# Kernel tuning notes

Measured on AMD Instinct MI355X. Metric: run time of the kernel, lower is better.

## Reference

```python
import jax, jax.numpy as jnp
import numpy as np

N_ATOMS = 10000
N_PAIRS = 320000
C = 64        # channel width (pp_nodes[-1], ii_nodes[-1], pi_nodes[-1])
NB = 10       # n_basis
EPS = 1e-3    # torsion-boost epsilon


def setup_inputs() -> dict:
    key = jax.random.key(0)
    ks = jax.random.split(key, 24)
    f32 = jnp.float32

    def w(k, shp):
        return jax.random.normal(k, shp, f32) / np.float32(np.sqrt(shp[0]))

    ind_2 = jax.random.randint(ks[0], (N_PAIRS, 2), 0, N_ATOMS)
    p1 = jax.random.normal(ks[1], (N_ATOMS, C), f32)
    p3 = jax.random.normal(ks[2], (N_ATOMS, 3, C), f32)
    basis = jax.random.uniform(ks[3], (N_PAIRS, NB), dtype=f32)
    d3 = jax.random.normal(ks[4], (N_PAIRS, 3), f32)
    d3 = d3 / jnp.linalg.norm(d3, axis=-1, keepdims=True)  # unit bond directions
    fc_edge = jax.random.uniform(ks[5], (N_PAIRS, 1), dtype=f32)  # cutoff in [0,1]

    return {
        'ind_2': ind_2, 'p1': p1, 'p3': p3, 'basis': basis, 'd3': d3, 'fc_edge': fc_edge,
        'pp_pre_W1': w(ks[6], (C, C)), 'pp_pre_b1': jnp.zeros((C,), f32),
        'pp_pre_W2': w(ks[7], (C, C)), 'pp_pre_b2': jnp.zeros((C,), f32),
        'pi_W': w(ks[8], (2 * C, C * NB)), 'pi_b': jnp.zeros((C * NB,), f32),
        'ii_W': w(ks[9], (C, 2 * C)),
        'pp_post_W1': w(ks[10], (2 * C, C)), 'pp_post_W2': w(ks[11], (C, C)),
        'eq_pp_W': w(ks[12], (C, C)),
        'pp1_W1': w(ks[13], (2 * C, C)), 'pp1_b1': jnp.zeros((C,), f32),
        'pp1_W2': w(ks[14], (C, 2 * C)), 'pp1_b2': jnp.zeros((2 * C,), f32),
    }


def _gc_block(ind_2, p1, p3, basis, d3, fc_edge,
              pp_pre_W1, pp_pre_b1, pp_pre_W2, pp_pre_b2,
              pi_W, pi_b, ii_W, pp_post_W1, pp_post_W2,
              eq_pp_W, pp1_W1, pp1_b1, pp1_W2, pp1_b2):
    n_atoms = p1.shape[0]
    i = ind_2[:, 0]
    j = ind_2[:, 1]

    # ---- InvarLayer ----
    # pp_pre: FF [C,C], tanh, bias
    p1_in = jnp.tanh(jnp.tanh(p1 @ pp_pre_W1 + pp_pre_b1) @ pp_pre_W2 + pp_pre_b2)
    # PILayer: concat(p1[i], p1[j]) -> Dense(C*NB) -> contract with radial basis
    pair = jnp.concatenate([p1_in[i], p1_in[j]], axis=-1)            # (P, 2C)
    h = jnp.tanh(pair @ pi_W + pi_b).reshape(-1, C, NB)              # (P, C, NB)
    i_pair = jnp.einsum('pcb,pb->pc', h, basis)                      # (P, C)
    # ii: FF [2C] (doubled for n_props=2), tanh, no bias
    i_pair = jnp.tanh(i_pair @ ii_W)                                 # (P, 2C)
    # IP: scatter-add onto receiver atom i
    p1_scat = jax.ops.segment_sum(i_pair, i, num_segments=n_atoms)   # (N, 2C)
    # pp_post: FF [C,C], tanh, no bias
    p1_new = jnp.tanh(jnp.tanh(p1_scat @ pp_post_W1) @ pp_post_W2)   # (N, C)

    i1a, i1b = jnp.split(i_pair, 2, axis=-1)  # chunks; rank-3 branch uses i1s[1]

    # ---- torsion boost (compute_torsion_boost_t3) ----
    v = jax.ops.segment_sum(d3 * fc_edge, i, num_segments=n_atoms)   # (N, 3)
    v_i = v[i]
    proj = jnp.sum(v_i * d3, axis=-1, keepdims=True)
    w = v_i - proj * d3                                              # perpendicular part
    w2 = jnp.sum(w * w, axis=-1, keepdims=True)
    g_deg = w2 / (w2 + (10.0 * EPS) ** 2)
    t3 = w * jax.lax.rsqrt(w2 + EPS * EPS) * g_deg                   # (P, 3)
    tb_gate = g_deg * (fc_edge * fc_edge)                            # (P, 1)

    # ---- EquivarLayer ----
    gate = i1b[:, None, :]                                           # (P, 1, C)
    ix = p3[j] * gate + d3[:, :, None] * gate \
         + t3[:, :, None] * (i1b * tb_gate)[:, None, :]              # (P, 3, C)
    p3_new = jax.ops.segment_sum(ix, i, num_segments=n_atoms)        # (N, 3, C)
    p3_new = p3_new @ eq_pp_W                                        # PP: no bias, no act
    dotted = jnp.einsum('ixr,ixr->ir', p3_new, p3_new)               # (N, C)

    # ---- output PP + gating ----
    h2 = jnp.tanh(jnp.concatenate([p1_new, dotted], axis=-1) @ pp1_W1 + pp1_b1)
    h2 = jnp.tanh(h2 @ pp1_W2 + pp1_b2)                              # (N, 2C)
    g1, g3 = jnp.split(h2, 2, axis=-1)
    p1_out = g1                                                      # (N, C)
    p3_out = p3_new * g3[:, None, :]                                 # ScaleLayer
    return p1_out, p3_out


def reference(ind_2, p1, p3, basis, d3, fc_edge,
              pp_pre_W1, pp_pre_b1, pp_pre_W2, pp_pre_b2,
              pi_W, pi_b, ii_W, pp_post_W1, pp_post_W2,
              eq_pp_W, pp1_W1, pp1_b1, pp1_W2, pp1_b2):
    return _gc_block(ind_2, p1, p3, basis, d3, fc_edge,
                     pp_pre_W1, pp_pre_b1, pp_pre_W2, pp_pre_b2,
                     pi_W, pi_b, ii_W, pp_post_W1, pp_post_W2,
                     eq_pp_W, pp1_W1, pp1_b1, pp1_W2, pp1_b2)
```

## Files before the change

kernel.cpp:

```cpp
#include <hip/hip_runtime.h>
#include <hip/hip_bf16.h>

#define N_ATOMS 10000
#define N_PAIRS 320000
#define C_ 64
#define NB_ 10

typedef short bf16x8 __attribute__((ext_vector_type(8)));
typedef float f32x4 __attribute__((ext_vector_type(4)));

__device__ __forceinline__ float bf2f(__hip_bfloat16 x) { return __bfloat162float(x); }
__device__ __forceinline__ float ldf(const void* p, int i, int isf32) {
    return isf32 ? ((const float*)p)[i] : bf2f(((const __hip_bfloat16*)p)[i]);
}
__device__ __forceinline__ short f2bs(float x) {
    __hip_bfloat16 h = __float2bfloat16(x);
    return *reinterpret_cast<short*>(&h);
}
__device__ __forceinline__ float bs2f(unsigned short s) {
    return __uint_as_float(((unsigned)s) << 16);
}
__device__ __forceinline__ float tanh_fast(float x) {
    const float e = __expf(2.0f * x);
    return 1.0f - 2.0f * __builtin_amdgcn_rcpf(e + 1.0f);
}

#define W_PPREW1 0
#define W_PPREB1 4096
#define W_PPREW2 4160
#define W_PPREB2 8256
#define W_PIW    8320
#define W_PIB    90240
#define W_IIW    90880
#define W_PPOSTW1 99072
#define W_PPOSTW2 107264
#define W_EQW    111360
#define W_Q1W    115456
#define W_Q1B    123648
#define W_Q2W    123712
#define W_Q2B    131904
#define W_TOTAL  132032

__global__ void k_probe(const void* __restrict__ d3, int* __restrict__ flag)
{
    if (threadIdx.x == 0 && blockIdx.x == 0) {
        float sf = 0.f, sb = 0.f;
        const float* f = (const float*)d3;
        const __hip_bfloat16* b = (const __hip_bfloat16*)d3;
        for (int r = 0; r < 4; r++) {
            float x = f[r*3], y = f[r*3+1], z = f[r*3+2];
            float n = x*x + y*y + z*z;
            sf += isfinite(n) ? fabsf(n - 1.f) : 1e30f;
            float xb = bf2f(b[r*3]), yb = bf2f(b[r*3+1]), zb = bf2f(b[r*3+2]);
            float nb = xb*xb + yb*yb + zb*zb;
            sb += isfinite(nb) ? fabsf(nb - 1.f) : 1e30f;
        }
        *flag = (sf < sb) ? 1 : 0;
    }
}

__global__ __launch_bounds__(256) void k_convert(
    const void* s0, const void* s1, const void* s2, const void* s3,
    const void* s4, const void* s5, const void* s6, const void* s7,
    const void* s8, const void* s9, const void* s10, const void* s11,
    const void* s12, const void* s13,
    float* __restrict__ wbuf, const int* __restrict__ flagp)
{
    const int idx = blockIdx.x * 256 + threadIdx.x;
    if (idx >= W_TOTAL) return;
    const int isf32 = *flagp;
    const int offs[15] = {W_PPREW1, W_PPREB1, W_PPREW2, W_PPREB2, W_PIW, W_PIB,
                          W_IIW, W_PPOSTW1, W_PPOSTW2, W_EQW, W_Q1W, W_Q1B,
                          W_Q2W, W_Q2B, W_TOTAL};
    const void* srcs[14] = {s0,s1,s2,s3,s4,s5,s6,s7,s8,s9,s10,s11,s12,s13};
    int t = 0;
    while (idx >= offs[t + 1]) t++;
    wbuf[idx] = ldf(srcs[t], idx - offs[t], isf32);
}

__global__ __launch_bounds__(256) void k_pack(
    const float* __restrict__ wbuf,
    short* __restrict__ piWBh, short* __restrict__ piWBl,
    short* __restrict__ iiWh, short* __restrict__ iiWl)
{
    int idx = blockIdx.x * 256 + threadIdx.x;
    if (idx < 81920) {
        const int j = idx & 7, lane = (idx >> 3) & 63, s = (idx >> 9) & 3, T = idx >> 11;
        const int k = s * 32 + (lane >> 4) * 8 + j;
        const int colp = T * 16 + (lane & 15);
        const int b = colp >> 6, c = colp & 63;
        const float v = wbuf[W_PIW + k * 640 + c * 10 + b];
        const short hs = f2bs(v);
        piWBh[idx] = hs;
        piWBl[idx] = f2bs(v - bs2f((unsigned short)hs));
        return;
    }
    idx -= 81920;
    if (idx < 8192) {
        const int j = idx & 7, lane = (idx >> 3) & 63, s2 = (idx >> 9) & 1, ct = idx >> 10;
        const int k = s2 * 32 + (lane >> 4) * 8 + j;
        const int col = ct * 16 + (lane & 15);
        const float wv = wbuf[W_IIW + k * 128 + col];
        const short hs = f2bs(wv);
        iiWh[idx] = hs;
        iiWl[idx] = f2bs(wv - bs2f((unsigned short)hs));
    }
}

__global__ __launch_bounds__(256) void k_p1in(
    const void* __restrict__ p1, const float* __restrict__ wbuf,
    const int* __restrict__ flagp,
    unsigned short* __restrict__ p1h, unsigned short* __restrict__ p1l)
{
    const float* W1 = wbuf + W_PPREW1;
    const float* b1 = wbuf + W_PPREB1;
    const float* W2 = wbuf + W_PPREW2;
    const float* b2 = wbuf + W_PPREB2;
    const int isf32 = *flagp;
    __shared__ float x[4][C_];
    __shared__ float h[4][C_];
    const int t = threadIdx.x;
    const int slot = t >> 6, c = t & 63;
    const int atom = blockIdx.x * 4 + slot;
    x[slot][c] = ldf(p1, atom * C_ + c, isf32);
    __syncthreads();
    float acc = b1[c];
    for (int k = 0; k < C_; k++) acc += x[slot][k] * W1[k * C_ + c];
    h[slot][c] = tanh_fast(acc);
    __syncthreads();
    acc = b2[c];
    for (int k = 0; k < C_; k++) acc += h[slot][k] * W2[k * C_ + c];
    const float f = tanh_fast(acc);
    const short hs = f2bs(f);
    p1h[atom * C_ + c] = (unsigned short)hs;
    p1l[atom * C_ + c] = (unsigned short)f2bs(f - bs2f((unsigned short)hs));
}

__global__ __launch_bounds__(256) void k_hist(const int* __restrict__ ind2, int* __restrict__ cnt)
{
    const int p = blockIdx.x * 256 + threadIdx.x;
    if (p < N_PAIRS) atomicAdd(&cnt[ind2[2 * p]], 1);
}
__global__ __launch_bounds__(256) void k_scan(const int* __restrict__ cnt, int* __restrict__ offs)
{
    __shared__ int part[256];
    __shared__ int base[257];
    const int t = threadIdx.x;
    const int lo = t * 40, hi = (lo + 40 < N_ATOMS) ? lo + 40 : N_ATOMS;
    int s = 0;
    for (int b = lo; b < hi; b++) s += cnt[b];
    part[t] = s;
    __syncthreads();
    if (t == 0) {
        int run = 0;
        for (int i = 0; i < 256; i++) { base[i] = run; run += part[i]; }
        base[256] = run;
    }
    __syncthreads();
    int run = base[t];
    for (int b = lo; b < hi; b++) { offs[b] = run; run += cnt[b]; }
    if (t == 0) offs[N_ATOMS] = base[256];
}
__global__ __launch_bounds__(256) void k_cpcur(const int* __restrict__ offs, int* __restrict__ cur)
{
    const int i = blockIdx.x * 256 + threadIdx.x;
    if (i < N_ATOMS) cur[i] = offs[i];
}
__global__ __launch_bounds__(256) void k_scatter(const int* __restrict__ ind2,
                                                 int* __restrict__ cur, int* __restrict__ perm)
{
    const int p = blockIdx.x * 256 + threadIdx.x;
    if (p >= N_PAIRS) return;
    const int pos = atomicAdd(&cur[ind2[2 * p]], 1);
    perm[pos] = p;
}

__global__ __launch_bounds__(256) void k_vscat(
    const int* __restrict__ ind2, const void* __restrict__ d3,
    const void* __restrict__ fc, const int* __restrict__ flagp, float* __restrict__ v)
{
    const int p = blockIdx.x * 256 + threadIdx.x;
    if (p >= N_PAIRS) return;
    const int isf32 = *flagp;
    const int ia = ind2[2 * p];
    const float f = ldf(fc, p, isf32);
    atomicAdd(&v[ia * 3 + 0], ldf(d3, p * 3 + 0, isf32) * f);
    atomicAdd(&v[ia * 3 + 1], ldf(d3, p * 3 + 1, isf32) * f);
    atomicAdd(&v[ia * 3 + 2], ldf(d3, p * 3 + 2, isf32) * f);
}

template<int FULLMODE>
__global__ __launch_bounds__(256) void k_pairs_t(
    const int* __restrict__ ind2, const void* __restrict__ basis,
    const void* __restrict__ d3, const void* __restrict__ fc,
    const void* __restrict__ p3,
    const float* __restrict__ wbuf,
    const short* __restrict__ piWBh, const short* __restrict__ piWBl,
    const short* __restrict__ iiWh, const short* __restrict__ iiWl,
    const unsigned short* __restrict__ p1h, const unsigned short* __restrict__ p1l,
    const int* __restrict__ flagp, const float* __restrict__ vglob,
    float* __restrict__ outA, float* __restrict__ outB)
{
    __shared__ __align__(16) unsigned short Bbuf[8192];
    __shared__ __align__(16) char SH[17408];
    __shared__ float basisL[640];
    __shared__ int sIL[64], sJL[64];
    __shared__ float d3L[64][3], t3L[64][3], tbL[64];

    float* preL = (float*)SH;
    float* i1bL = (float*)SH;

    const int t = threadIdx.x;
    const int P0 = blockIdx.x * 64;
    const int isf32 = *flagp;
    const int lane = t & 63;
    const int w = t >> 6;
    const int lc = lane & 15;
    const int quad = lane >> 4;

    if (t < 64) {
        int2 ij = ((const int2*)ind2)[P0 + t];
        sIL[t] = ij.x; sJL[t] = ij.y;
    }
    for (int e = t; e < 640; e += 256) basisL[e] = ldf(basis, P0 * 10 + e, isf32);
    __syncthreads();

    bf16x8 ah[4], al[4];
    {
        const int ia = sIL[w * 16 + lc];
        const int ja = sJL[w * 16 + lc];
        #pragma unroll
        for (int s = 0; s < 4; s++) {
            const int atom = (s < 2) ? ia : ja;
            const int off = atom * 64 + (s & 1) * 32 + quad * 8;
            ah[s] = *(const bf16x8*)(p1h + off);
            al[s] = *(const bf16x8*)(p1l + off);
        }
    }

    float sr[4][4];
    #pragma unroll
    for (int r = 0; r < 4; r++)
        #pragma unroll
        for (int ph = 0; ph < 4; ph++) sr[r][ph] = 0.f;

    for (int cc = 0; cc < 10; cc++) {
        f32x4 acc[4];
        #pragma unroll
        for (int tt = 0; tt < 4; tt++) acc[tt] = (f32x4){0.f, 0.f, 0.f, 0.f};

        __syncthreads();
        {
            const uint4* gsrc = (const uint4*)(piWBh + cc * 8192);
            uint4* ldst = (uint4*)Bbuf;
            #pragma unroll
            for (int r = 0; r < 4; r++) ldst[r * 256 + t] = gsrc[r * 256 + t];
        }
        __syncthreads();
        #pragma unroll
        for (int tt = 0; tt < 4; tt++) {
            #pragma unroll
            for (int s = 0; s < 4; s++) {
                bf16x8 bfr = *(const bf16x8*)&Bbuf[((tt * 4 + s) * 64 + lane) * 8];
                acc[tt] = __builtin_amdgcn_mfma_f32_16x16x32_bf16(ah[s], bfr, acc[tt], 0, 0, 0);
                acc[tt] = __builtin_amdgcn_mfma_f32_16x16x32_bf16(al[s], bfr, acc[tt], 0, 0, 0);
            }
        }
        __syncthreads();
        {
            const uint4* gsrc = (const uint4*)(piWBl + cc * 8192);
            uint4* ldst = (uint4*)Bbuf;
            #pragma unroll
            for (int r = 0; r < 4; r++) ldst[r * 256 + t] = gsrc[r * 256 + t];
        }
        __syncthreads();
        #pragma unroll
        for (int tt = 0; tt < 4; tt++) {
            #pragma unroll
            for (int s = 0; s < 4; s++) {
                bf16x8 bfr = *(const bf16x8*)&Bbuf[((tt * 4 + s) * 64 + lane) * 8];
                acc[tt] = __builtin_amdgcn_mfma_f32_16x16x32_bf16(ah[s], bfr, acc[tt], 0, 0, 0);
            }
            const int c = tt * 16 + lc;
            const float bias = wbuf[W_PIB + c * 10 + cc];
            #pragma unroll
            for (int r = 0; r < 4; r++) {
                const int m = w * 16 + quad * 4 + r;
                const float h = tanh_fast(acc[tt][r] + bias);
                sr[r][tt] += h * basisL[m * 10 + cc];
            }
        }
    }

    #pragma unroll
    for (int r = 0; r < 4; r++)
        #pragma unroll
        for (int ph = 0; ph < 4; ph++)
            preL[(w * 16 + quad * 4 + r) * 68 + ph * 16 + lc] = sr[r][ph];
    __syncthreads();

    bf16x8 ah2[2], al2[2];
    {
        const int row = w * 16 + lc;
        #pragma unroll
        for (int s2 = 0; s2 < 2; s2++) {
            const float* pr2 = &preL[row * 68 + s2 * 32 + quad * 8];
            #pragma unroll
            for (int j = 0; j < 8; j++) {
                const float x = pr2[j];
                const short hs = f2bs(x);
                ah2[s2][j] = hs;
                al2[s2][j] = f2bs(x - bs2f((unsigned short)hs));
            }
        }
    }
    __syncthreads();

    #pragma unroll
    for (int ct = 0; ct < 8; ct++) {
        f32x4 acc = {0.f, 0.f, 0.f, 0.f};
        #pragma unroll
        for (int s2 = 0; s2 < 2; s2++) {
            bf16x8 bh = *(const bf16x8*)&iiWh[((ct * 2 + s2) * 64 + lane) * 8];
            bf16x8 bl = *(const bf16x8*)&iiWl[((ct * 2 + s2) * 64 + lane) * 8];
            acc = __builtin_amdgcn_mfma_f32_16x16x32_bf16(ah2[s2], bh, acc, 0, 0, 0);
            acc = __builtin_amdgcn_mfma_f32_16x16x32_bf16(al2[s2], bh, acc, 0, 0, 0);
            acc = __builtin_amdgcn_mfma_f32_16x16x32_bf16(ah2[s2], bl, acc, 0, 0, 0);
        }
        const int ch = ct * 16 + lc;
        if (FULLMODE) {
            #pragma unroll
            for (int r = 0; r < 4; r++) {
                const int m = w * 16 + quad * 4 + r;
                outA[(size_t)(P0 + m) * 128 + ch] = tanh_fast(acc[r]);
            }
        } else {
            #pragma unroll
            for (int r = 0; r < 4; r++) {
                const int m = w * 16 + quad * 4 + r;
                const float val = tanh_fast(acc[r]);
                atomicAdd(&outA[(size_t)sIL[m] * 128 + ch], val);
                if (ch >= 64) i1bL[m * 64 + (ch - 64)] = val;
            }
        }
    }

    if (!FULLMODE) {
        __syncthreads();
        if (t < 64) {
            const int m = t;
            const int ia = sIL[m];
            const float vi0 = vglob[ia * 3 + 0], vi1 = vglob[ia * 3 + 1], vi2 = vglob[ia * 3 + 2];
            const float d0 = ldf(d3, (P0 + m) * 3 + 0, isf32);
            const float d1 = ldf(d3, (P0 + m) * 3 + 1, isf32);
            const float d2 = ldf(d3, (P0 + m) * 3 + 2, isf32);
            d3L[m][0] = d0; d3L[m][1] = d1; d3L[m][2] = d2;
            const float proj = vi0 * d0 + vi1 * d1 + vi2 * d2;
            const float w0 = vi0 - proj * d0, w1 = vi1 - proj * d1, w2v = vi2 - proj * d2;
            const float w2 = w0 * w0 + w1 * w1 + w2v * w2v;
            const float g = w2 / (w2 + 1e-4f);
            const float rs = rsqrtf(w2 + 1e-6f);
            t3L[m][0] = w0 * rs * g; t3L[m][1] = w1 * rs * g; t3L[m][2] = w2v * rs * g;
            const float f = ldf(fc, P0 + m, isf32);
            tbL[m] = g * f * f;
        }
        __syncthreads();
        const int c = lane;
        #pragma unroll 4
        for (int mm = 0; mm < 16; mm++) {
            const int m = w * 16 + mm;
            const float bv = i1bL[m * 64 + c];
            const float coef = bv * tbL[m];
            #pragma unroll
            for (int x = 0; x < 3; x++) {
                const float p3v = ldf(p3, sJL[m] * 192 + x * 64 + c, isf32);
                atomicAdd(&outB[(size_t)sIL[m] * 192 + x * 64 + c],
                          p3v * bv + d3L[m][x] * bv + t3L[m][x] * coef);
            }
        }
    }
}

__global__ __launch_bounds__(64) void k_reduce(
    const int* __restrict__ ind2, const void* __restrict__ d3,
    const void* __restrict__ fc, const void* __restrict__ p3,
    const float* __restrict__ ip, const int* __restrict__ perm,
    const int* __restrict__ offs, const float* __restrict__ wbuf,
    const int* __restrict__ flagp, void* __restrict__ out)
{
    const int a = blockIdx.x;
    const int l = threadIdx.x;
    const int isf32 = *flagp;
    const int q0 = offs[a], q1 = offs[a + 1];

    float vx = 0.f, vy = 0.f, vz = 0.f;
    for (int q = q0 + l; q < q1; q += 64) {
        const int p = perm[q];
        const float f = ldf(fc, p, isf32);
        vx += ldf(d3, 3 * p + 0, isf32) * f;
        vy += ldf(d3, 3 * p + 1, isf32) * f;
        vz += ldf(d3, 3 * p + 2, isf32) * f;
    }
    #pragma unroll
    for (int off = 32; off; off >>= 1) {
        vx += __shfl_xor(vx, off);
        vy += __shfl_xor(vy, off);
        vz += __shfl_xor(vz, off);
    }

    float accA = 0.f, accB = 0.f, a30 = 0.f, a31 = 0.f, a32 = 0.f;
    #pragma unroll 2
    for (int q = q0; q < q1; q++) {
        const int p = perm[q];
        const float f = ldf(fc, p, isf32);
        const float d0 = ldf(d3, 3 * p + 0, isf32);
        const float d1 = ldf(d3, 3 * p + 1, isf32);
        const float d2 = ldf(d3, 3 * p + 2, isf32);
        const float proj = vx * d0 + vy * d1 + vz * d2;
        const float w0 = vx - proj * d0, w1 = vy - proj * d1, w2v = vz - proj * d2;
        const float w2 = w0 * w0 + w1 * w1 + w2v * w2v;
        const float g = w2 / (w2 + 1e-4f);
        const float rs = rsqrtf(w2 + 1e-6f);
        const float t30 = w0 * rs * g, t31 = w1 * rs * g, t32 = w2v * rs * g;
        const float tb = g * f * f;
        const int jj = ind2[2 * p + 1];
        const float ipa = ip[(size_t)p * 128 + l];
        const float ipb = ip[(size_t)p * 128 + 64 + l];
        accA += ipa; accB += ipb;
        const float coef = ipb * tb;
        a30 += ldf(p3, jj * 192 + l, isf32) * ipb + d0 * ipb + t30 * coef;
        a31 += ldf(p3, jj * 192 + 64 + l, isf32) * ipb + d1 * ipb + t31 * coef;
        a32 += ldf(p3, jj * 192 + 128 + l, isf32) * ipb + d2 * ipb + t32 * coef;
    }

    __shared__ float s1m[128];
    __shared__ float p3s[192];
    __shared__ float hA[64];
    __shared__ float cat[128];
    __shared__ float hB[64];
    s1m[l] = accA; s1m[64 + l] = accB;
    p3s[l] = a30; p3s[64 + l] = a31; p3s[128 + l] = a32;
    __syncthreads();

    const float* ppW1 = wbuf + W_PPOSTW1;
    const float* ppW2 = wbuf + W_PPOSTW2;
    const float* eqW  = wbuf + W_EQW;
    const float* q1W  = wbuf + W_Q1W;
    const float* q1b  = wbuf + W_Q1B;
    const float* q2W  = wbuf + W_Q2W;
    const float* q2b  = wbuf + W_Q2B;

    float acc = 0.f;
    for (int k = 0; k < 128; k++) acc += s1m[k] * ppW1[k * 64 + l];
    hA[l] = tanh_fast(acc);
    __syncthreads();
    acc = 0.f;
    for (int k = 0; k < 64; k++) acc += hA[k] * ppW2[k * 64 + l];
    const float p1n = tanh_fast(acc);

    float pn0 = 0.f, pn1 = 0.f, pn2 = 0.f;
    for (int k = 0; k < 64; k++) {
        const float e = eqW[k * 64 + l];
        pn0 += p3s[k] * e;
        pn1 += p3s[64 + k] * e;
        pn2 += p3s[128 + k] * e;
    }
    cat[l] = p1n;
    cat[64 + l] = pn0 * pn0 + pn1 * pn1 + pn2 * pn2;
    __syncthreads();

    acc = q1b[l];
    for (int k = 0; k < 128; k++) acc += cat[k] * q1W[k * 64 + l];
    hB[l] = tanh_fast(acc);
    __syncthreads();

    float g1 = q2b[l], g3 = q2b[64 + l];
    for (int k = 0; k < 64; k++) {
        const float hv = hB[k];
        g1 += hv * q2W[k * 128 + l];
        g3 += hv * q2W[k * 128 + 64 + l];
    }
    g1 = tanh_fast(g1);
    g3 = tanh_fast(g3);

    if (isf32) {
        float* p1o = (float*)out;
        float* p3o = p1o + 640000;
        p1o[a * 64 + l] = g1;
        p3o[a * 192 + l] = pn0 * g3;
        p3o[a * 192 + 64 + l] = pn1 * g3;
        p3o[a * 192 + 128 + l] = pn2 * g3;
    } else {
        __hip_bfloat16* p1o = (__hip_bfloat16*)out;
        __hip_bfloat16* p3o = p1o + 640000;
        p1o[a * 64 + l] = __float2bfloat16(g1);
        p3o[a * 192 + l] = __float2bfloat16(pn0 * g3);
        p3o[a * 192 + 64 + l] = __float2bfloat16(pn1 * g3);
        p3o[a * 192 + 128 + l] = __float2bfloat16(pn2 * g3);
    }
}

__global__ __launch_bounds__(256) void k_final(
    const float* __restrict__ p1scat, const float* __restrict__ p3acc,
    const float* __restrict__ wbuf, const int* __restrict__ flagp,
    void* __restrict__ out)
{
    const float* ppW1 = wbuf + W_PPOSTW1;
    const float* ppW2 = wbuf + W_PPOSTW2;
    const float* eqW  = wbuf + W_EQW;
    const float* q1W  = wbuf + W_Q1W;
    const float* q1b  = wbuf + W_Q1B;
    const float* q2W  = wbuf + W_Q2W;
    const float* q2b  = wbuf + W_Q2B;
    const int isf32 = *flagp;

    __shared__ float s1[4][128];
    __shared__ float hA[4][64];
    __shared__ float cat[4][128];
    __shared__ float p3a[4][192];
    const int t = threadIdx.x;
    const int slot = t >> 6, c = t & 63;
    const int atom = blockIdx.x * 4 + slot;

    s1[slot][c]        = p1scat[atom * 128 + c];
    s1[slot][64 + c]   = p1scat[atom * 128 + 64 + c];
    p3a[slot][c]       = p3acc[atom * 192 + c];
    p3a[slot][64 + c]  = p3acc[atom * 192 + 64 + c];
    p3a[slot][128 + c] = p3acc[atom * 192 + 128 + c];
    __syncthreads();

    float acc = 0.f;
    for (int k = 0; k < 128; k++) acc += s1[slot][k] * ppW1[k * 64 + c];
    hA[slot][c] = tanh_fast(acc);
    __syncthreads();
    acc = 0.f;
    for (int k = 0; k < 64; k++) acc += hA[slot][k] * ppW2[k * 64 + c];
    cat[slot][c] = tanh_fast(acc);

    float pn[3];
    float dot = 0.f;
    #pragma unroll
    for (int x = 0; x < 3; x++) {
        float a = 0.f;
        for (int k = 0; k < 64; k++) a += p3a[slot][x * 64 + k] * eqW[k * 64 + c];
        pn[x] = a;
        dot += a * a;
    }
    cat[slot][64 + c] = dot;
    __syncthreads();

    acc = q1b[c];
    for (int k = 0; k < 128; k++) acc += cat[slot][k] * q1W[k * 64 + c];
    __syncthreads();
    hA[slot][c] = tanh_fast(acc);
    __syncthreads();

    float g1acc = q2b[c], g3acc = q2b[c + 64];
    for (int k = 0; k < 64; k++) {
        const float hv = hA[slot][k];
        g1acc += hv * q2W[k * 128 + c];
        g3acc += hv * q2W[k * 128 + c + 64];
    }
    const float g1 = tanh_fast(g1acc);
    const float g3 = tanh_fast(g3acc);
    if (isf32) {
        float* p1o = (float*)out;
        float* p3o = p1o + 640000;
        p1o[atom * 64 + c] = g1;
        #pragma unroll
        for (int x = 0; x < 3; x++) p3o[atom * 192 + x * 64 + c] = pn[x] * g3;
    } else {
        __hip_bfloat16* p1o = (__hip_bfloat16*)out;
        __hip_bfloat16* p3o = p1o + 640000;
        p1o[atom * 64 + c] = __float2bfloat16(g1);
        #pragma unroll
        for (int x = 0; x < 3; x++) p3o[atom * 192 + x * 64 + c] = __float2bfloat16(pn[x] * g3);
    }
}

extern "C" void kernel_launch(void* const* d_in, const int* in_sizes, int n_in,
                              void* d_out, int out_size, void* d_ws, size_t ws_size,
                              hipStream_t stream)
{
    const int* ind2 = (const int*)d_in[0];
    const void* p1    = d_in[1];
    const void* p3    = d_in[2];
    const void* basis = d_in[3];
    const void* d3    = d_in[4];
    const void* fc    = d_in[5];

    char* W = (char*)d_ws;
    float* wbuf  = (float*)(W + 0);
    short* piWBh = (short*)(W + 528128);
    short* piWBl = (short*)(W + 691968);
    short* iiWh  = (short*)(W + 855808);
    short* iiWl  = (short*)(W + 872192);
    unsigned short* p1h = (unsigned short*)(W + 888576);
    unsigned short* p1l = (unsigned short*)(W + 2168576);
    int* flag = (int*)(W + 3448576);

    const int full = (ws_size >= 168688704ULL) ? 1 : 0;

    k_probe<<<1, 64, 0, stream>>>(d3, flag);
    k_convert<<<516, 256, 0, stream>>>(
        d_in[6], d_in[7], d_in[8], d_in[9], d_in[10], d_in[11], d_in[12],
        d_in[13], d_in[14], d_in[15], d_in[16], d_in[17], d_in[18], d_in[19],
        wbuf, flag);
    k_pack<<<352, 256, 0, stream>>>(wbuf, piWBh, piWBl, iiWh, iiWl);
    k_p1in<<<2500, 256, 0, stream>>>(p1, wbuf, flag, p1h, p1l);

    if (full) {
        int* cnt  = (int*)(W + 3448640);
        int* offs = (int*)(W + 3488640);
        int* cur  = (int*)(W + 3528704);
        int* perm = (int*)(W + 3568704);
        float* ip = (float*)(W + 4848704);

        hipMemsetAsync(cnt, 0, 40000, stream);
        k_hist<<<1250, 256, 0, stream>>>(ind2, cnt);
        k_scan<<<1, 256, 0, stream>>>(cnt, offs);
        k_cpcur<<<40, 256, 0, stream>>>(offs, cur);
        k_scatter<<<1250, 256, 0, stream>>>(ind2, cur, perm);
        k_pairs_t<1><<<5000, 256, 0, stream>>>(ind2, basis, d3, fc, p3,
                                               wbuf, piWBh, piWBl, iiWh, iiWl,
                                               p1h, p1l, flag, nullptr,
                                               ip, nullptr);
        k_reduce<<<10000, 64, 0, stream>>>(ind2, d3, fc, p3, ip, perm, offs,
                                           wbuf, flag, d_out);
    } else {
        float* v      = (float*)(W + 3448640);
        float* p1scat = (float*)(W + 3568640);
        float* p3acc  = (float*)(W + 8688640);

        hipMemsetAsync(v, 0, 120000 + 5120000 + 7680000, stream);
        k_vscat<<<1250, 256, 0, stream>>>(ind2, d3, fc, flag, v);
        k_pairs_t<0><<<5000, 256, 0, stream>>>(ind2, basis, d3, fc, p3,
                                               wbuf, piWBh, piWBl, iiWh, iiWl,
                                               p1h, p1l, flag, v,
                                               p1scat, p3acc);
        k_final<<<2500, 256, 0, stream>>>(p1scat, p3acc, wbuf, flag, d_out);
    }
}
```

Before: 525.8 us.

## Sort pairs by atom and fuse pair MLP with segmented scatter-reduce

Pair data (indices, basis, d3, fc) is gathered into atom-sorted order. A separate kernel reduces the per-atom torsion vector. A fused pair kernel then computes the pair MLP and does a segmented in-block reduction of consecutive same-atom pairs before issuing atomics into per-atom accumulators, followed by the existing k_final. This removes the large per-pair intermediate buffer (P×128 floats) and the per-atom sequential reduce kernel, and cuts atomic traffic. In exchange it adds a gather pass and a memset of the accumulators, and lowers the workspace threshold needed to take this path.

Measured after the change: 597.5 us. +13.6%, slower.

```diff
diff --git a/kernel.cpp b/kernel.cpp
--- a/kernel.cpp
+++ b/kernel.cpp
@@ -175,18 +175,232 @@
     perm[pos] = p;
 }
 
-__global__ __launch_bounds__(256) void k_vscat(
-    const int* __restrict__ ind2, const void* __restrict__ d3,
-    const void* __restrict__ fc, const int* __restrict__ flagp, float* __restrict__ v)
-{
-    const int p = blockIdx.x * 256 + threadIdx.x;
-    if (p >= N_PAIRS) return;
+__global__ __launch_bounds__(256) void k_gatherperm(
+    const int* __restrict__ ind2, const void* __restrict__ basis,
+    const void* __restrict__ d3, const void* __restrict__ fc,
+    const int* __restrict__ perm, const int* __restrict__ flagp,
+    int* __restrict__ ind2P, float* __restrict__ basisP,
+    float* __restrict__ d3P, float* __restrict__ fcP)
+{
+    const int q = blockIdx.x * 256 + threadIdx.x;
+    if (q >= N_PAIRS) return;
     const int isf32 = *flagp;
-    const int ia = ind2[2 * p];
-    const float f = ldf(fc, p, isf32);
-    atomicAdd(&v[ia * 3 + 0], ldf(d3, p * 3 + 0, isf32) * f);
-    atomicAdd(&v[ia * 3 + 1], ldf(d3, p * 3 + 1, isf32) * f);
-    atomicAdd(&v[ia * 3 + 2], ldf(d3, p * 3 + 2, isf32) * f);
+    const int p = perm[q];
+    ((int2*)ind2P)[q] = ((const int2*)ind2)[p];
+    fcP[q] = ldf(fc, p, isf32);
+    #pragma unroll
+    for (int x = 0; x < 3; x++) d3P[3 * q + x] = ldf(d3, 3 * p + x, isf32);
+    #pragma unroll
+    for (int b = 0; b < 10; b++) basisP[10 * q + b] = ldf(basis, 10 * p + b, isf32);
+}
+
+__global__ __launch_bounds__(64) void k_vred(
+    const float* __restrict__ d3P, const float* __restrict__ fcP,
+    const int* __restrict__ offs, float* __restrict__ v)
+{
+    const int a = blockIdx.x;
+    const int l = threadIdx.x;
+    const int q0 = offs[a], q1 = offs[a + 1];
+    float vx = 0.f, vy = 0.f, vz = 0.f;
+    for (int q = q0 + l; q < q1; q += 64) {
+        const float f = fcP[q];
+        vx += d3P[3 * q + 0] * f;
+        vy += d3P[3 * q + 1] * f;
+        vz += d3P[3 * q + 2] * f;
+    }
+    #pragma unroll
+    for (int off = 32; off; off >>= 1) {
+        vx += __shfl_xor(vx, off);
+        vy += __shfl_xor(vy, off);
+        vz += __shfl_xor(vz, off);
+    }
+    if (l == 0) { v[a * 3 + 0] = vx; v[a * 3 + 1] = vy; v[a * 3 + 2] = vz; }
+}
+
+__global__ __launch_bounds__(256) void k_pairs_fused(
+    const int* __restrict__ ind2P, const float* __restrict__ basisP,
+    const float* __restrict__ d3P, const float* __restrict__ fcP,
+    const void* __restrict__ p3,
+    const float* __restrict__ wbuf,
+    const short* __restrict__ piWBh, const short* __restrict__ piWBl,
+    const short* __restrict__ iiWh, const short* __restrict__ iiWl,
+    const unsigned short* __restrict__ p1h, const unsigned short* __restrict__ p1l,
+    const int* __restrict__ flagp, const float* __restrict__ vglob,
+    float* __restrict__ p1scat, float* __restrict__ p3acc)
+{
+    __shared__ __align__(16) char SH[36352];
+    __shared__ int sIL[64], sJL[64];
+    __shared__ float d3L[64][3], t3L[64][3], tbL[64];
+
+    unsigned short* Bbuf = (unsigned short*)SH;
+    float* preL   = (float*)(SH + 16384);
+    float* ipL    = (float*)SH;
+    float* basisL = (float*)(SH + 33792);
+
+    const int t = threadIdx.x;
+    const int P0 = blockIdx.x * 64;
+    const int isf32 = *flagp;
+    const int lane = t & 63;
+    const int w = t >> 6;
+    const int lc = lane & 15;
+    const int quad = lane >> 4;
+
+    if (t < 64) {
+        int2 ij = ((const int2*)ind2P)[P0 + t];
+        sIL[t] = ij.x; sJL[t] = ij.y;
+        const float vi0 = vglob[ij.x * 3 + 0], vi1 = vglob[ij.x * 3 + 1], vi2 = vglob[ij.x * 3 + 2];
+        const float d0 = d3P[(P0 + t) * 3 + 0];
+        const float d1 = d3P[(P0 + t) * 3 + 1];
+        const float d2 = d3P[(P0 + t) * 3 + 2];
+        d3L[t][0] = d0; d3L[t][1] = d1; d3L[t][2] = d2;
+        const float proj = vi0 * d0 + vi1 * d1 + vi2 * d2;
+        const float w0 = vi0 - proj * d0, w1 = vi1 - proj * d1, w2v = vi2 - proj * d2;
+        const float w2 = w0 * w0 + w1 * w1 + w2v * w2v;
+        const float g = w2 / (w2 + 1e-4f);
+        const float rs = rsqrtf(w2 + 1e-6f);
+        t3L[t][0] = w0 * rs * g; t3L[t][1] = w1 * rs * g; t3L[t][2] = w2v * rs * g;
+        const float f = fcP[P0 + t];
+        tbL[t] = g * f * f;
+    }
+    for (int e = t; e < 640; e += 256) basisL[e] = basisP[P0 * 10 + e];
+    __syncthreads();
+
+    bf16x8 ah[4], al[4];
+    {
+        const int ia = sIL[w * 16 + lc];
+        const int ja = sJL[w * 16 + lc];
+        #pragma unroll
+        for (int s = 0; s < 4; s++) {
+            const int atom = (s < 2) ? ia : ja;
+            const int off = atom * 64 + (s & 1) * 32 + quad * 8;
+            ah[s] = *(const bf16x8*)(p1h + off);
+            al[s] = *(const bf16x8*)(p1l + off);
+        }
+    }
+
+    float sr[4][4];
+    #pragma unroll
+    for (int r = 0; r < 4; r++)
+        #pragma unroll
+        for (int ph = 0; ph < 4; ph++) sr[r][ph] = 0.f;
+
+    for (int cc = 0; cc < 10; cc++) {
+        f32x4 acc[4];
+        #pragma unroll
+        for (int tt = 0; tt < 4; tt++) acc[tt] = (f32x4){0.f, 0.f, 0.f, 0.f};
+
+        __syncthreads();
+        {
+            const uint4* gsrc = (const uint4*)(piWBh + cc * 8192);
+            uint4* ldst = (uint4*)Bbuf;
+            #pragma unroll
+            for (int r = 0; r < 4; r++) ldst[r * 256 + t] = gsrc[r * 256 + t];
+        }
+        __syncthreads();
+        #pragma unroll
+        for (int tt = 0; tt < 4; tt++) {
+            #pragma unroll
+            for (int s = 0; s < 4; s++) {
+                bf16x8 bfr = *(const bf16x8*)&Bbuf[((tt * 4 + s) * 64 + lane) * 8];
+                acc[tt] = __builtin_amdgcn_mfma_f32_16x16x32_bf16(ah[s], bfr, acc[tt], 0, 0, 0);
+                acc[tt] = __builtin_amdgcn_mfma_f32_16x16x32_bf16(al[s], bfr, acc[tt], 0, 0, 0);
+            }
+        }
+        __syncthreads();
+        {
+            const uint4* gsrc = (const uint4*)(piWBl + cc * 8192);
+            uint4* ldst = (uint4*)Bbuf;
+            #pragma unroll
+            for (int r = 0; r < 4; r++) ldst[r * 256 + t] = gsrc[r * 256 + t];
+        }
+        __syncthreads();
+        #pragma unroll
+        for (int tt = 0; tt < 4; tt++) {
+            #pragma unroll
+            for (int s = 0; s < 4; s++) {
+                bf16x8 bfr = *(const bf16x8*)&Bbuf[((tt * 4 + s) * 64 + lane) * 8];
+                acc[tt] = __builtin_amdgcn_mfma_f32_16x16x32_bf16(ah[s], bfr, acc[tt], 0, 0, 0);
+            }
+            const int c = tt * 16 + lc;
+            const float bias = wbuf[W_PIB + c * 10 + cc];
+            #pragma unroll
+            for (int r = 0; r < 4; r++) {
+                const int m = w * 16 + quad * 4 + r;
+                const float h = tanh_fast(acc[tt][r] + bias);
+                sr[r][tt] += h * basisL[m * 10 + cc];
+            }
+        }
+    }
+
+    #pragma unroll
+    for (int r = 0; r < 4; r++)
+        #pragma unroll
+        for (int ph = 0; ph < 4; ph++)
+            preL[(w * 16 + quad * 4 + r) * 68 + ph * 16 + lc] = sr[r][ph];
+    __syncthreads();
+
+    bf16x8 ah2[2], al2[2];
+    {
+        const int row = w * 16 + lc;
+        #pragma unroll
+        for (int s2 = 0; s2 < 2; s2++) {
+            const float* pr2 = &preL[row * 68 + s2 * 32 + quad * 8];
+            #pragma unroll
+            for (int j = 0; j < 8; j++) {
+                const float x = pr2[j];
+                const short hs = f2bs(x);
+                ah2[s2][j] = hs;
+                al2[s2][j] = f2bs(x - bs2f((unsigned short)hs));
+            }
+        }
+    }
+    __syncthreads();
+
+    #pragma unroll
+    for (int ct = 0; ct < 8; ct++) {
+        f32x4 acc = {0.f, 0.f, 0.f, 0.f};
+        #pragma unroll
+        for (int s2 = 0; s2 < 2; s2++) {
+            bf16x8 bh = *(const bf16x8*)&iiWh[((ct * 2 + s2) * 64 + lane) * 8];
+            bf16x8 bl = *(const bf16x8*)&iiWl[((ct * 2 + s2) * 64 + lane) * 8];
+            acc = __builtin_amdgcn_mfma_f32_16x16x32_bf16(ah2[s2], bh, acc, 0, 0, 0);
+            acc = __builtin_amdgcn_mfma_f32_16x16x32_bf16(al2[s2], bh, acc, 0, 0, 0);
+            acc = __builtin_amdgcn_mfma_f32_16x16x32_bf16(ah2[s2], bl, acc, 0, 0, 0);
+        }
+        const int ch = ct * 16 + lc;
+        #pragma unroll
+        for (int r = 0; r < 4; r++) {
+            const int m = w * 16 + quad * 4 + r;
+            ipL[m * 130 + ch] = tanh_fast(acc[r]);
+        }
+    }
+    __syncthreads();
+
+    if (t < 128) {
+        float acc = 0.f;
+        #pragma unroll 4
+        for (int m = 0; m < 64; m++) {
+            acc += ipL[m * 130 + t];
+            if (m == 63 || sIL[m + 1] != sIL[m]) {
+                atomicAdd(&p1scat[(size_t)sIL[m] * 128 + t], acc);
+                acc = 0.f;
+            }
+        }
+    }
+    if (t < 192) {
+        const int x = t >> 6, cc = t & 63;
+        float acc = 0.f;
+        #pragma unroll 4
+        for (int m = 0; m < 64; m++) {
+            const float ipb = ipL[m * 130 + 64 + cc];
+            const float p3v = ldf(p3, sJL[m] * 192 + t, isf32);
+            acc += (p3v + d3L[m][x]) * ipb + t3L[m][x] * (ipb * tbL[m]);
+            if (m == 63 || sIL[m + 1] != sIL[m]) {
+                atomicAdd(&p3acc[(size_t)sIL[m] * 192 + t], acc);
+                acc = 0.f;
+            }
+        }
+    }
 }
 
 template<int FULLMODE>
@@ -381,125 +595,6 @@
     }
 }
 
-__global__ __launch_bounds__(64) void k_reduce(
-    const int* __restrict__ ind2, const void* __restrict__ d3,
-    const void* __restrict__ fc, const void* __restrict__ p3,
-    const float* __restrict__ ip, const int* __restrict__ perm,
-    const int* __restrict__ offs, const float* __restrict__ wbuf,
-    const int* __restrict__ flagp, void* __restrict__ out)
-{
-    const int a = blockIdx.x;
-    const int l = threadIdx.x;
-    const int isf32 = *flagp;
-    const int q0 = offs[a], q1 = offs[a + 1];
-
-    float vx = 0.f, vy = 0.f, vz = 0.f;
-    for (int q = q0 + l; q < q1; q += 64) {
-        const int p = perm[q];
-        const float f = ldf(fc, p, isf32);
-        vx += ldf(d3, 3 * p + 0, isf32) * f;
-        vy += ldf(d3, 3 * p + 1, isf32) * f;
-        vz += ldf(d3, 3 * p + 2, isf32) * f;
-    }
-    #pragma unroll
-    for (int off = 32; off; off >>= 1) {
-        vx += __shfl_xor(vx, off);
-        vy += __shfl_xor(vy, off);
-        vz += __shfl_xor(vz, off);
-    }
-
-    float accA = 0.f, accB = 0.f, a30 = 0.f, a31 = 0.f, a32 = 0.f;
-    #pragma unroll 2
-    for (int q = q0; q < q1; q++) {
-        const int p = perm[q];
-        const float f = ldf(fc, p, isf32);
-        const float d0 = ldf(d3, 3 * p + 0, isf32);
-        const float d1 = ldf(d3, 3 * p + 1, isf32);
-        const float d2 = ldf(d3, 3 * p + 2, isf32);
-        const float proj = vx * d0 + vy * d1 + vz * d2;
-        const float w0 = vx - proj * d0, w1 = vy - proj * d1, w2v = vz - proj * d2;
-        const float w2 = w0 * w0 + w1 * w1 + w2v * w2v;
-        const float g = w2 / (w2 + 1e-4f);
-        const float rs = rsqrtf(w2 + 1e-6f);
-        const float t30 = w0 * rs * g, t31 = w1 * rs * g, t32 = w2v * rs * g;
-        const float tb = g * f * f;
-        const int jj = ind2[2 * p + 1];
-        const float ipa = ip[(size_t)p * 128 + l];
-        const float ipb = ip[(size_t)p * 128 + 64 + l];
-        accA += ipa; accB += ipb;
-        const float coef = ipb * tb;
-        a30 += ldf(p3, jj * 192 + l, isf32) * ipb + d0 * ipb + t30 * coef;
-        a31 += ldf(p3, jj * 192 + 64 + l, isf32) * ipb + d1 * ipb + t31 * coef;
-        a32 += ldf(p3, jj * 192 + 128 + l, isf32) * ipb + d2 * ipb + t32 * coef;
-    }
-
-    __shared__ float s1m[128];
-    __shared__ float p3s[192];
-    __shared__ float hA[64];
-    __shared__ float cat[128];
-    __shared__ float hB[64];
-    s1m[l] = accA; s1m[64 + l] = accB;
-    p3s[l] = a30; p3s[64 + l] = a31; p3s[128 + l] = a32;
-    __syncthreads();
-
-    const float* ppW1 = wbuf + W_PPOSTW1;
-    const float* ppW2 = wbuf + W_PPOSTW2;
-    const float* eqW  = wbuf + W_EQW;
-    const float* q1W  = wbuf + W_Q1W;
-    const float* q1b  = wbuf + W_Q1B;
-    const float* q2W  = wbuf + W_Q2W;
-    const float* q2b  = wbuf + W_Q2B;
-
-    float acc = 0.f;
-    for (int k = 0; k < 128; k++) acc += s1m[k] * ppW1[k * 64 + l];
-    hA[l] = tanh_fast(acc);
-    __syncthreads();
-    acc = 0.f;
-    for (int k = 0; k < 64; k++) acc += hA[k] * ppW2[k * 64 + l];
-    const float p1n = tanh_fast(acc);
-
-    float pn0 = 0.f, pn1 = 0.f, pn2 = 0.f;
-    for (int k = 0; k < 64; k++) {
-        const float e = eqW[k * 64 + l];
-        pn0 += p3s[k] * e;
-        pn1 += p3s[64 + k] * e;
-        pn2 += p3s[128 + k] * e;
-    }
-    cat[l] = p1n;
-    cat[64 + l] = pn0 * pn0 + pn1 * pn1 + pn2 * pn2;
-    __syncthreads();
-
-    acc = q1b[l];
-    for (int k = 0; k < 128; k++) acc += cat[k] * q1W[k * 64 + l];
-    hB[l] = tanh_fast(acc);
-    __syncthreads();
-
-    float g1 = q2b[l], g3 = q2b[64 + l];
-    for (int k = 0; k < 64; k++) {
-        const float hv = hB[k];
-        g1 += hv * q2W[k * 128 + l];
-        g3 += hv * q2W[k * 128 + 64 + l];
-    }
-    g1 = tanh_fast(g1);
-    g3 = tanh_fast(g3);
-
-    if (isf32) {
-        float* p1o = (float*)out;
-        float* p3o = p1o + 640000;
-        p1o[a * 64 + l] = g1;
-        p3o[a * 192 + l] = pn0 * g3;
-        p3o[a * 192 + 64 + l] = pn1 * g3;
-        p3o[a * 192 + 128 + l] = pn2 * g3;
-    } else {
-        __hip_bfloat16* p1o = (__hip_bfloat16*)out;
-        __hip_bfloat16* p3o = p1o + 640000;
-        p1o[a * 64 + l] = __float2bfloat16(g1);
-        p3o[a * 192 + l] = __float2bfloat16(pn0 * g3);
-        p3o[a * 192 + 64 + l] = __float2bfloat16(pn1 * g3);
-        p3o[a * 192 + 128 + l] = __float2bfloat16(pn2 * g3);
-    }
-}
-
 __global__ __launch_bounds__(256) void k_final(
     const float* __restrict__ p1scat, const float* __restrict__ p3acc,
     const float* __restrict__ wbuf, const int* __restrict__ flagp,
@@ -576,6 +671,20 @@
         #pragma unroll
         for (int x = 0; x < 3; x++) p3o[atom * 192 + x * 64 + c] = __float2bfloat16(pn[x] * g3);
     }
+}
+
+__global__ __launch_bounds__(256) void k_vscat(
+    const int* __restrict__ ind2, const void* __restrict__ d3,
+    const void* __restrict__ fc, const int* __restrict__ flagp, float* __restrict__ v)
+{
+    const int p = blockIdx.x * 256 + threadIdx.x;
+    if (p >= N_PAIRS) return;
+    const int isf32 = *flagp;
+    const int ia = ind2[2 * p];
+    const float f = ldf(fc, p, isf32);
+    atomicAdd(&v[ia * 3 + 0], ldf(d3, p * 3 + 0, isf32) * f);
+    atomicAdd(&v[ia * 3 + 1], ldf(d3, p * 3 + 1, isf32) * f);
+    atomicAdd(&v[ia * 3 + 2], ldf(d3, p * 3 + 2, isf32) * f);
 }
 
 extern "C" void kernel_launch(void* const* d_in, const int* in_sizes, int n_in,
@@ -599,7 +708,7 @@
     unsigned short* p1l = (unsigned short*)(W + 2168576);
     int* flag = (int*)(W + 3448576);
 
-    const int full = (ws_size >= 168688704ULL) ? 1 : 0;
+    const int fused = (ws_size >= 38248704ULL) ? 1 : 0;
 
     k_probe<<<1, 64, 0, stream>>>(d3, flag);
     k_convert<<<516, 256, 0, stream>>>(
@@ -609,24 +718,32 @@
     k_pack<<<352, 256, 0, stream>>>(wbuf, piWBh, piWBl, iiWh, iiWl);
     k_p1in<<<2500, 256, 0, stream>>>(p1, wbuf, flag, p1h, p1l);
 
-    if (full) {
-        int* cnt  = (int*)(W + 3448640);
-        int* offs = (int*)(W + 3488640);
-        int* cur  = (int*)(W + 3528704);
-        int* perm = (int*)(W + 3568704);
-        float* ip = (float*)(W + 4848704);
+    if (fused) {
+        int* cnt      = (int*)(W + 3448640);
+        int* offs     = (int*)(W + 3488640);
+        int* cur      = (int*)(W + 3528704);
+        int* perm     = (int*)(W + 3568704);
+        int* ind2P    = (int*)(W + 4848704);
+        float* basisP = (float*)(W + 7408704);
+        float* d3P    = (float*)(W + 20208704);
+        float* fcP    = (float*)(W + 24048704);
+        float* v      = (float*)(W + 25328704);
+        float* p1scat = (float*)(W + 25448704);
+        float* p3acc  = (float*)(W + 30568704);
 
         hipMemsetAsync(cnt, 0, 40000, stream);
+        hipMemsetAsync(p1scat, 0, 5120000 + 7680000, stream);
         k_hist<<<1250, 256, 0, stream>>>(ind2, cnt);
         k_scan<<<1, 256, 0, stream>>>(cnt, offs);
         k_cpcur<<<40, 256, 0, stream>>>(offs, cur);
         k_scatter<<<1250, 256, 0, stream>>>(ind2, cur, perm);
-        k_pairs_t<1><<<5000, 256, 0, stream>>>(ind2, basis, d3, fc, p3,
-                                               wbuf, piWBh, piWBl, iiWh, iiWl,
-                                               p1h, p1l, flag, nullptr,
-                                               ip, nullptr);
-        k_reduce<<<10000, 64, 0, stream>>>(ind2, d3, fc, p3, ip, perm, offs,
-                                           wbuf, flag, d_out);
+        k_gatherperm<<<1250, 256, 0, stream>>>(ind2, basis, d3, fc, perm, flag,
+                                               ind2P, basisP, d3P, fcP);
+        k_vred<<<10000, 64, 0, stream>>>(d3P, fcP, offs, v);
+        k_pairs_fused<<<5000, 256, 0, stream>>>(ind2P, basisP, d3P, fcP, p3,
+                                                wbuf, piWBh, piWBl, iiWh, iiWl,
+                                                p1h, p1l, flag, v, p1scat, p3acc);
+        k_final<<<2500, 256, 0, stream>>>(p1scat, p3acc, wbuf, flag, d_out);
     } else {
         float* v      = (float*)(W + 3448640);
         float* p1scat = (float*)(W + 3568640);
```
